# Kernel optimization log

Measured on AMD Instinct MI355X. Metric: run time of the kernel, lower is better.

## Reference

```python
import jax, jax.numpy as jnp
import numpy as np

WH, WW = 7, 7           # window height/width
N = WH * WW             # tokens per window = 49
C = 768                 # num_channels
H = 24                  # num_heads
D = C // H              # head_dim = 32
B = 1024                # total windows (batch * windows-per-image)
NW = 64                 # windows per image (shift_mask leading dim)
EPS = 1e-5


def _relative_position_index():
    # Mirrors the torch buffer construction in __init__.
    coords = np.stack(np.meshgrid(np.arange(WH), np.arange(WW), indexing='ij'))  # [2,WH,WW]
    cf = coords.reshape(2, -1)                          # [2,N]
    rel = cf[:, :, None] - cf[:, None, :]               # [2,N,N]
    rel = rel.transpose(1, 2, 0).copy()                 # [N,N,2]
    rel[:, :, 0] += WH - 1
    rel[:, :, 1] += WW - 1
    rel[:, :, 0] *= 2 * WW - 1
    return jnp.asarray(rel.sum(-1), dtype=jnp.int32)    # [N,N]


def setup_inputs() -> dict:
    key = jax.random.key(0)
    ks = jax.random.split(key, 6)
    x = jax.random.normal(ks[0], (B, N, C), dtype=jnp.float32)
    shift_mask = jax.random.normal(ks[1], (NW, N, N), dtype=jnp.float32)
    w_qkv = jax.random.normal(ks[2], (3 * C, C), dtype=jnp.float32) * 0.02
    b_qkv = jnp.zeros((3 * C,), dtype=jnp.float32)
    w_proj = jax.random.normal(ks[3], (C, C), dtype=jnp.float32) * 0.02
    b_proj = jnp.zeros((C,), dtype=jnp.float32)
    rel_bias_table = jax.random.normal(ks[4], ((2 * WH - 1) * (2 * WW - 1), H), dtype=jnp.float32) * 0.02
    ln_g = jnp.ones((C,), dtype=jnp.float32)
    ln_b = jnp.zeros((C,), dtype=jnp.float32)
    rel_pos_index = _relative_position_index()
    return {
        'x': x, 'shift_mask': shift_mask,
        'w_qkv': w_qkv, 'b_qkv': b_qkv,
        'w_proj': w_proj, 'b_proj': b_proj,
        'rel_bias_table': rel_bias_table,
        'ln_g': ln_g, 'ln_b': ln_b,
        'rel_pos_index': rel_pos_index,
    }


def reference(x, shift_mask, w_qkv, b_qkv, w_proj, b_proj, rel_bias_table, ln_g, ln_b, rel_pos_index):
    B_, N_, C_ = x.shape
    # QKV projection: [B,N,3C] -> [3,B,H,N,D]
    qkv = (x @ w_qkv.T + b_qkv).reshape(B_, N_, 3, H, D).transpose(2, 0, 3, 1, 4)
    q, k, v = qkv[0], qkv[1], qkv[2]
    # Relative position bias gather: [N,N,H] -> [1,H,N,N]
    bias = rel_bias_table[rel_pos_index.reshape(-1)].reshape(N_, N_, H).transpose(2, 0, 1)[None]
    # Shift mask broadcast over batch repeats and heads: [B,1,N,N]
    mask = jnp.tile(shift_mask, (B_ // shift_mask.shape[0], 1, 1))[:, None]
    attn_bias = bias + mask  # [B,H,N,N]
    scale = 1.0 / np.sqrt(D).astype(np.float32)
    scores = jnp.einsum('bhnd,bhmd->bhnm', q, k) * scale + attn_bias
    attn = jax.nn.softmax(scores, axis=-1)
    out = jnp.einsum('bhnm,bhmd->bhnd', attn, v)       # [B,H,N,D]
    out = out.transpose(0, 2, 1, 3).reshape(B_, N_, C_)
    out = out @ w_proj.T + b_proj                      # dropout p=0 -> identity
    y = out + x
    mu = jnp.mean(y, axis=-1, keepdims=True)
    var = jnp.mean(jnp.square(y - mu), axis=-1, keepdims=True)
    return (y - mu) * jax.lax.rsqrt(var + EPS) * ln_g + ln_b
```

## Files before the change

### kernel.cpp

```cpp
#include <hip/hip_runtime.h>
#include <hip/hip_bf16.h>

#define SEQ 49
#define CH 768
#define NH 24
#define HD 32
#define NB 1024
#define NWIN 64
#define MTOT (NB*SEQ)

typedef __hip_bfloat16 bf16;
typedef __attribute__((ext_vector_type(8))) short short8;
typedef __attribute__((ext_vector_type(4))) short short4v;
typedef __attribute__((ext_vector_type(4))) float f32x4;

#define MD  ((size_t)MTOT * HD)
#define NHMD ((size_t)NH * MD)

__device__ __forceinline__ void gload16(const void* g, void* l) {
  __builtin_amdgcn_global_load_lds((__attribute__((address_space(1))) void*)g,
                                   (__attribute__((address_space(3))) void*)l,
                                   16, 0, 0);
}

__device__ __forceinline__ float bf2f(short s) {
  return __uint_as_float(((unsigned int)(unsigned short)s) << 16);
}

__global__ void cvt_bf16(const float* __restrict__ in, bf16* __restrict__ o, int n4) {
  int i = blockIdx.x * blockDim.x + threadIdx.x;
  if (i >= n4) return;
  float4 v = ((const float4*)in)[i];
  union { bf16 b[4]; short4 s; } u;
  u.b[0] = __float2bfloat16(v.x);
  u.b[1] = __float2bfloat16(v.y);
  u.b[2] = __float2bfloat16(v.z);
  u.b[3] = __float2bfloat16(v.w);
  ((short4*)o)[i] = u.s;
}

__global__ void build_comb(const float* __restrict__ table, const int* __restrict__ rpi,
                           const float* __restrict__ smask, bf16* __restrict__ comb) {
  int i = blockIdx.x * blockDim.x + threadIdx.x;
  if (i >= NWIN * NH * 1024) return;
  int idx = i * 4;
  int e0 = idx & 7;
  int l = (idx >> 3) & 63;
  int jj = (idx >> 9) & 7;
  int sh = idx >> 12;
  int h = sh % NH;
  int s = sh / NH;
  union { bf16 b[4]; short4 v; } u;
#pragma unroll
  for (int k = 0; k < 4; k++) {
    int j = jj * 8 + e0 + k;
    int mt = j >> 4, nt = (j >> 2) & 3, r = j & 3;
    int m = 16 * mt + 4 * (l >> 4) + r;
    int n = 16 * nt + (l & 15);
    float v = -1e30f;
    if (m < SEQ && n < SEQ)
      v = (table[rpi[m * SEQ + n] * NH + h] + smask[s * SEQ * SEQ + m * SEQ + n])
          * 1.4426950408889634f;
    u.b[k] = __float2bfloat16(v);
  }
  *(short4*)(comb + idx) = u.v;
}

__global__ __launch_bounds__(512) void qkv_gemm(
    const bf16* __restrict__ A, const bf16* __restrict__ Bw,
    const float* __restrict__ bias, bf16* __restrict__ C)
{
  extern __shared__ __align__(16) bf16 lds[];
  const int tid = threadIdx.x;
  const int w = tid >> 6, l = tid & 63;
  const int lr = l & 15, lg = l >> 4;
  const int wm = w >> 2, wn = w & 3;

  const int flat = blockIdx.x;
  const int xcd = flat & 7, lid = flat >> 3;
  const int wgid = (xcd < 4 ? xcd * 221 : 884 + (xcd - 4) * 220) + lid;
  const int bm = wgid / 9, bn = wgid - 9 * bm;

  const bf16* gA[4];
  const bf16* gB[4];
  int ldst[4];
#pragma unroll
  for (int j = 0; j < 4; j++) {
    int c = j * 512 + tid;
    int row = c >> 3, cpos = c & 7;
    int srcch = cpos ^ (row & 7);
    gA[j] = A + ((size_t)(bm * 256 + row)) * CH + srcch * 8;
    gB[j] = Bw + ((size_t)(bn * 256 + row)) * CH + srcch * 8;
    ldst[j] = c * 8;
  }

  f32x4 acc[8][4];
  f32x4 zero4 = {0.f, 0.f, 0.f, 0.f};
#pragma unroll
  for (int i = 0; i < 8; i++)
#pragma unroll
    for (int j = 0; j < 4; j++) acc[i][j] = zero4;

  int offA[8][2], offB[4][2];
#pragma unroll
  for (int mi = 0; mi < 8; mi++)
#pragma unroll
    for (int ks = 0; ks < 2; ks++) {
      int rowa = wm * 128 + mi * 16 + lr;
      offA[mi][ks] = rowa * 64 + ((lg + 4 * ks) ^ (rowa & 7)) * 8;
    }
#pragma unroll
  for (int nj = 0; nj < 4; nj++)
#pragma unroll
    for (int ks = 0; ks < 2; ks++) {
      int rowb = wn * 64 + nj * 16 + lr;
      offB[nj][ks] = rowb * 64 + ((lg + 4 * ks) ^ (rowb & 7)) * 8;
    }

  gload16(gB[0], lds + 32768 + ldst[0]);
  gload16(gB[1], lds + 32768 + ldst[1]);
  gload16(gB[2], lds + 32768 + ldst[2]);
  gload16(gB[3], lds + 32768 + ldst[3]);
  gload16(gA[0], lds + ldst[0]);
  gload16(gA[2], lds + ldst[2]);
  gload16(gA[1], lds + ldst[1]);
  gload16(gA[3], lds + ldst[3]);

  for (int t = 0; t < 12; ++t) {
    const int cur = t & 1;
    const bf16* cA = lds + cur * 16384;
    const bf16* cB = lds + 32768 + cur * 16384;
    bf16* nA = lds + (cur ^ 1) * 16384;
    bf16* nB = lds + 32768 + (cur ^ 1) * 16384;
    const int kk = (t + 1) * 64;
    const bool pf = (t < 11);
#pragma unroll
    for (int p = 0; p < 4; ++p) {
      const int hp = p >> 1, ks = p & 1;
      if (p == 0) {
        asm volatile("s_waitcnt vmcnt(2)" ::: "memory");
      } else if (p == 2) {
        if (pf) asm volatile("s_waitcnt vmcnt(4)" ::: "memory");
        else    asm volatile("s_waitcnt vmcnt(0)" ::: "memory");
      }
      __builtin_amdgcn_sched_barrier(0);
      __builtin_amdgcn_s_barrier();
      __builtin_amdgcn_sched_barrier(0);
      short8 af[4], bfv[4];
#pragma unroll
      for (int mi = 0; mi < 4; mi++) af[mi] = *(const short8*)(cA + offA[hp * 4 + mi][ks]);
#pragma unroll
      for (int nj = 0; nj < 4; nj++) bfv[nj] = *(const short8*)(cB + offB[nj][ks]);
      if (pf) {
        if (p == 0) { gload16(gB[0] + kk, nB + ldst[0]); gload16(gB[1] + kk, nB + ldst[1]); }
        if (p == 1) { gload16(gB[2] + kk, nB + ldst[2]); gload16(gB[3] + kk, nB + ldst[3]); }
        if (p == 2) { gload16(gA[0] + kk, nA + ldst[0]); gload16(gA[2] + kk, nA + ldst[2]); }
        if (p == 3) { gload16(gA[1] + kk, nA + ldst[1]); gload16(gA[3] + kk, nA + ldst[3]); }
      }
      asm volatile("s_waitcnt lgkmcnt(0)" ::: "memory");
      __builtin_amdgcn_sched_barrier(0);
      __builtin_amdgcn_s_setprio(1);
#pragma unroll
      for (int mi = 0; mi < 4; mi++)
#pragma unroll
        for (int nj = 0; nj < 4; nj++)
          acc[hp * 4 + mi][nj] =
              __builtin_amdgcn_mfma_f32_16x16x32_bf16(af[mi], bfv[nj], acc[hp * 4 + mi][nj], 0, 0, 0);
      __builtin_amdgcn_s_setprio(0);
    }
  }

  const float scale = 0.25503487724583985f;
  const int colbase = bn * 256 + 64 * wn;
  const int rowbase = bm * 256 + 128 * wm;
#pragma unroll
  for (int nj = 0; nj < 4; nj++) {
    const int cb16 = colbase + 16 * nj;
    const int sec = cb16 / 768;
    const int rem = cb16 - sec * 768;
    const int h = rem >> 5;
    const int dbase = rem & 31;
    float bv = bias[cb16 + lr];
    if (sec == 2) {
      const size_t vbase = 2 * NHMD + ((size_t)h * HD + dbase + lr) * MTOT;
#pragma unroll
      for (int mi = 0; mi < 8; mi++) {
        size_t row = rowbase + 16 * mi + 4 * lg;
        union { bf16 b[4]; short4 s; } u;
#pragma unroll
        for (int r = 0; r < 4; r++) u.b[r] = __float2bfloat16(acc[mi][nj][r] + bv);
        *(short4*)(C + vbase + row) = u.s;
      }
    } else {
      const float mul = (sec == 0) ? scale : 1.0f;
      const size_t base = (size_t)sec * NHMD + (size_t)h * MD + dbase + lr;
#pragma unroll
      for (int mi = 0; mi < 8; mi++) {
#pragma unroll
        for (int r = 0; r < 4; r++) {
          size_t row = rowbase + 16 * mi + 4 * lg + r;
          C[base + row * HD] = __float2bfloat16((acc[mi][nj][r] + bv) * mul);
        }
      }
    }
  }
}

__global__ __launch_bounds__(256, 3) void attn_kernel(
    const bf16* __restrict__ qkvT, const bf16* __restrict__ comb,
    bf16* __restrict__ aout)
{
  __shared__ __align__(16) bf16 P[4][64 * 72];
  const int tid = threadIdx.x;
  const int w = tid >> 6, l = tid & 63;
  const int lr = l & 15, lg = l >> 4;
  const int b = blockIdx.x;
  const int h = blockIdx.y * 4 + w;
  const size_t rowb = (size_t)b * SEQ;
  f32x4 zero4 = {0.f, 0.f, 0.f, 0.f};

  const bf16* qb = qkvT + (size_t)h * MD + rowb * HD;
  const bf16* kb = qkvT + NHMD + (size_t)h * MD + rowb * HD;
  const bf16* vT = qkvT + 2 * NHMD + (size_t)h * HD * MTOT;

  short8 qf[4], kf[4];
#pragma unroll
  for (int mt = 0; mt < 4; mt++)
    qf[mt] = *(const short8*)(qb + (16 * mt + lr) * HD + 8 * lg);
#pragma unroll
  for (int nt = 0; nt < 4; nt++)
    kf[nt] = *(const short8*)(kb + (16 * nt + lr) * HD + 8 * lg);

  f32x4 s[4][4];
#pragma unroll
  for (int mt = 0; mt < 4; mt++)
#pragma unroll
    for (int nt = 0; nt < 4; nt++)
      s[mt][nt] = __builtin_amdgcn_mfma_f32_16x16x32_bf16(qf[mt], kf[nt], zero4, 0, 0, 0);

  short8 pb[2][2];
#pragma unroll
  for (int kt = 0; kt < 2; kt++)
#pragma unroll
    for (int dt = 0; dt < 2; dt++)
      pb[kt][dt] = *(const short8*)(vT + ((size_t)(16 * dt + lr)) * MTOT + rowb + 32 * kt + 8 * lg);

  const bf16* cbp = comb + (((size_t)(b & (NWIN - 1)) * NH + h) << 12);
  short8 c8[8];
#pragma unroll
  for (int jj = 0; jj < 8; jj++)
    c8[jj] = *(const short8*)(cbp + (jj * 64 + l) * 8);
#pragma unroll
  for (int jj = 0; jj < 8; jj++)
#pragma unroll
    for (int e = 0; e < 8; e++)
      s[jj >> 1][(jj & 1) * 2 + (e >> 2)][e & 3] += bf2f(c8[jj][e]);

  float inv[4][4];
#pragma unroll
  for (int mt = 0; mt < 4; mt++)
#pragma unroll
    for (int r = 0; r < 4; r++) {
      float t = 0.f;
#pragma unroll
      for (int nt = 0; nt < 4; nt++) {
        float e = exp2f(s[mt][nt][r]);
        s[mt][nt][r] = e;
        t += e;
      }
      t += __shfl_xor(t, 1, 64);
      t += __shfl_xor(t, 2, 64);
      t += __shfl_xor(t, 4, 64);
      t += __shfl_xor(t, 8, 64);
      inv[mt][r] = 1.0f / t;
    }

#pragma unroll
  for (int mt = 0; mt < 4; mt++)
#pragma unroll
    for (int nt = 0; nt < 4; nt++)
#pragma unroll
      for (int r = 0; r < 4; r++)
        P[w][(16 * mt + 4 * lg + r) * 72 + 16 * nt + lr] =
            __float2bfloat16(s[mt][nt][r]);

  f32x4 o[4][2];
#pragma unroll
  for (int mt = 0; mt < 4; mt++) { o[mt][0] = zero4; o[mt][1] = zero4; }
#pragma unroll
  for (int kt = 0; kt < 2; kt++) {
    short8 pa[4];
#pragma unroll
    for (int mt = 0; mt < 4; mt++)
      pa[mt] = *(const short8*)(&P[w][(16 * mt + lr) * 72 + 32 * kt + 8 * lg]);
#pragma unroll
    for (int mt = 0; mt < 4; mt++)
#pragma unroll
      for (int dt = 0; dt < 2; dt++)
        o[mt][dt] = __builtin_amdgcn_mfma_f32_16x16x32_bf16(pa[mt], pb[kt][dt], o[mt][dt], 0, 0, 0);
  }

#pragma unroll
  for (int mt = 0; mt < 4; mt++)
#pragma unroll
    for (int dt = 0; dt < 2; dt++)
#pragma unroll
      for (int r = 0; r < 4; r++) {
        int m = 16 * mt + 4 * lg + r;
        if (m < SEQ)
          aout[(rowb + m) * CH + h * HD + 16 * dt + lr] =
              __float2bfloat16(o[mt][dt][r] * inv[mt][r]);
      }
}

__global__ __launch_bounds__(256) void proj_gemm(
    const bf16* __restrict__ A, const bf16* __restrict__ Bw,
    const float* __restrict__ bias, const bf16* __restrict__ xb,
    bf16* __restrict__ Y)
{
  __shared__ __align__(16) bf16 As[2 * 128 * 64];
  __shared__ __align__(16) bf16 Bs[2 * 128 * 64];
  const int tid = threadIdx.x;
  const int w = tid >> 6, l = tid & 63;
  const int lr = l & 15, lg = l >> 4;
  const int wm = w >> 1, wn = w & 1;

  const int flat = blockIdx.x;
  const int wg = (flat & 7) * 294 + (flat >> 3);
  const int bm = wg / 6, bn = wg - 6 * (wg / 6);

  const bf16* gA[4];
  const bf16* gB[4];
  int ldst[4];
#pragma unroll
  for (int j = 0; j < 4; j++) {
    int c = j * 256 + tid;
    int row = c >> 3, cpos = c & 7;
    int srcch = cpos ^ (row & 7);
    gA[j] = A + ((size_t)(bm * 128 + row)) * CH + srcch * 8;
    gB[j] = Bw + ((size_t)(bn * 128 + row)) * CH + srcch * 8;
    ldst[j] = c * 8;
  }

  f32x4 acc[4][4];
  f32x4 zero4 = {0.f, 0.f, 0.f, 0.f};
#pragma unroll
  for (int i = 0; i < 4; i++)
#pragma unroll
    for (int j = 0; j < 4; j++) acc[i][j] = zero4;

  int offA[4][2], offB[4][2];
#pragma unroll
  for (int mi = 0; mi < 4; mi++) {
#pragma unroll
    for (int ks = 0; ks < 2; ks++) {
      int rowa = 64 * wm + 16 * mi + lr;
      offA[mi][ks] = rowa * 64 + ((lg + 4 * ks) ^ (rowa & 7)) * 8;
      int rowb = 64 * wn + 16 * mi + lr;
      offB[mi][ks] = rowb * 64 + ((lg + 4 * ks) ^ (rowb & 7)) * 8;
    }
  }

#pragma unroll
  for (int j = 0; j < 4; j++) gload16(gA[j], As + ldst[j]);
#pragma unroll
  for (int j = 0; j < 4; j++) gload16(gB[j], Bs + ldst[j]);

  for (int t = 0; t < 12; ++t) {
    const int base = (t & 1) * 8192;
    asm volatile("s_waitcnt vmcnt(0)" ::: "memory");
    __builtin_amdgcn_sched_barrier(0);
    __builtin_amdgcn_s_barrier();
    __builtin_amdgcn_sched_barrier(0);
    const bf16* cA = As + base;
    const bf16* cB = Bs + base;
    bf16* nA = As + (base ^ 8192);
    bf16* nB = Bs + (base ^ 8192);
    const int kk = (t + 1) * 64;
    const bool pf = (t < 11);
#pragma unroll
    for (int ks = 0; ks < 2; ks++) {
      short8 af[4], bfv[4];
#pragma unroll
      for (int mi = 0; mi < 4; mi++) {
        af[mi] = *(const short8*)(cA + offA[mi][ks]);
        bfv[mi] = *(const short8*)(cB + offB[mi][ks]);
      }
      if (pf) {
#pragma unroll
        for (int j = 0; j < 2; j++) {
          gload16(gA[ks * 2 + j] + kk, nA + ldst[ks * 2 + j]);
          gload16(gB[ks * 2 + j] + kk, nB + ldst[ks * 2 + j]);
        }
      }
      asm volatile("s_waitcnt lgkmcnt(0)" ::: "memory");
      __builtin_amdgcn_sched_barrier(0);
      __builtin_amdgcn_s_setprio(1);
#pragma unroll
      for (int mi = 0; mi < 4; mi++)
#pragma unroll
        for (int nj = 0; nj < 4; nj++)
          acc[mi][nj] = __builtin_amdgcn_mfma_f32_16x16x32_bf16(af[mi], bfv[nj], acc[mi][nj], 0, 0, 0);
      __builtin_amdgcn_s_setprio(0);
    }
  }

  const int colbase = bn * 128 + 64 * wn;
  const int rowbase = bm * 128 + 64 * wm;
#pragma unroll
  for (int nj = 0; nj < 4; nj++) {
    int col = colbase + 16 * nj + lr;
    float bv = bias[col];
#pragma unroll
    for (int mi = 0; mi < 4; mi++) {
#pragma unroll
      for (int r = 0; r < 4; r++) {
        size_t row = rowbase + 16 * mi + 4 * lg + r;
        float v = acc[mi][nj][r] + bv + bf2f(((const short*)xb)[row * CH + col]);
        Y[row * CH + col] = __float2bfloat16(v);
      }
    }
  }
}

__global__ __launch_bounds__(256) void ln_kernel(
    const bf16* __restrict__ Y, const float* __restrict__ g,
    const float* __restrict__ be, float* __restrict__ out)
{
  const int w = threadIdx.x >> 6, l = threadIdx.x & 63;
  const size_t r = (size_t)blockIdx.x * 4 + w;
  const bf16* yr = Y + r * CH;

  short8 a = *(const short8*)(yr + 8 * l);
  short4v b4 = *(const short4v*)(yr + 512 + 4 * l);
  float v[12];
#pragma unroll
  for (int j = 0; j < 8; j++) v[j] = bf2f(a[j]);
#pragma unroll
  for (int j = 0; j < 4; j++) v[8 + j] = bf2f(b4[j]);

  float s1 = 0.f, s2 = 0.f;
#pragma unroll
  for (int j = 0; j < 12; j++) { s1 += v[j]; s2 += v[j] * v[j]; }
#pragma unroll
  for (int m = 1; m <= 32; m <<= 1) {
    s1 += __shfl_xor(s1, m, 64);
    s2 += __shfl_xor(s2, m, 64);
  }
  float mu = s1 * (1.0f / 768.0f);
  float var = s2 * (1.0f / 768.0f) - mu * mu;
  float rs = rsqrtf(var + 1e-5f);

  float4 g0 = *(const float4*)(g + 8 * l);
  float4 g1 = *(const float4*)(g + 8 * l + 4);
  float4 g2 = *(const float4*)(g + 512 + 4 * l);
  float4 b0 = *(const float4*)(be + 8 * l);
  float4 b1 = *(const float4*)(be + 8 * l + 4);
  float4 b2 = *(const float4*)(be + 512 + 4 * l);

  float4 o0, o1, o2;
  o0.x = (v[0] - mu) * rs * g0.x + b0.x;
  o0.y = (v[1] - mu) * rs * g0.y + b0.y;
  o0.z = (v[2] - mu) * rs * g0.z + b0.z;
  o0.w = (v[3] - mu) * rs * g0.w + b0.w;
  o1.x = (v[4] - mu) * rs * g1.x + b1.x;
  o1.y = (v[5] - mu) * rs * g1.y + b1.y;
  o1.z = (v[6] - mu) * rs * g1.z + b1.z;
  o1.w = (v[7] - mu) * rs * g1.w + b1.w;
  o2.x = (v[8] - mu) * rs * g2.x + b2.x;
  o2.y = (v[9] - mu) * rs * g2.y + b2.y;
  o2.z = (v[10] - mu) * rs * g2.z + b2.z;
  o2.w = (v[11] - mu) * rs * g2.w + b2.w;

  float* orow = out + r * CH;
  *(float4*)(orow + 8 * l) = o0;
  *(float4*)(orow + 8 * l + 4) = o1;
  *(float4*)(orow + 512 + 4 * l) = o2;
}

extern "C" void kernel_launch(void* const* d_in, const int* in_sizes, int n_in,
                              void* d_out, int out_size, void* d_ws, size_t ws_size,
                              hipStream_t stream) {
  (void)in_sizes; (void)n_in; (void)out_size; (void)ws_size;
  const float* x     = (const float*)d_in[0];
  const float* smask = (const float*)d_in[1];
  const float* wqkv  = (const float*)d_in[2];
  const float* bqkv  = (const float*)d_in[3];
  const float* wproj = (const float*)d_in[4];
  const float* bproj = (const float*)d_in[5];
  const float* table = (const float*)d_in[6];
  const float* lng   = (const float*)d_in[7];
  const float* lnb   = (const float*)d_in[8];
  const int*   rpi   = (const int*)d_in[9];
  float* out = (float*)d_out;

  char* ws = (char*)d_ws;
  bf16*  xb   = (bf16*)(ws);
  bf16*  wqb  = (bf16*)(ws + 77070336);
  bf16*  wpb  = (bf16*)(ws + 80609280);
  bf16*  comb = (bf16*)(ws + 81788928);
  bf16*  qkvT = (bf16*)(ws + 94371840);
  bf16*  aout = (bf16*)(ws + 325582848);
  bf16*  yb   = (bf16*)(ws + 94371840);

  cvt_bf16<<<37632, 256, 0, stream>>>(x, xb, 9633792);
  cvt_bf16<<<1728, 256, 0, stream>>>(wqkv, wqb, 442368);
  cvt_bf16<<<576, 256, 0, stream>>>(wproj, wpb, 147456);
  build_comb<<<6144, 256, 0, stream>>>(table, rpi, smask, comb);
  qkv_gemm<<<1764, 512, 131072, stream>>>(xb, wqb, bqkv, qkvT);
  attn_kernel<<<dim3(1024, 6), 256, 0, stream>>>(qkvT, comb, aout);
  proj_gemm<<<2352, 256, 0, stream>>>(aout, wpb, bproj, xb, yb);
  ln_kernel<<<12544, 256, 0, stream>>>(yb, lng, lnb, out);
}
```

Measured before the change: 520.3 us.

## Stream attention score tiles per row-block and issue all GEMM prefetches up front

The attention kernel now computes QK^T, adds the bias/mask, runs the softmax and writes P one 16-row tile at a time, instead of holding the full 4x4 score array in registers. The launch bound rises from 3 to 4 blocks per SM. The aim is lower register pressure so more waves can be resident. In the GEMM main loop, all eight next-tile global-to-LDS loads are now issued in the first k-substep rather than split across both, so they start earlier. The cost is more load/MFMA serialization inside each tile step and a burstier memory queue.

```diff
diff --git a/kernel.cpp b/kernel.cpp
--- a/kernel.cpp
+++ b/kernel.cpp
@@ -206,7 +206,7 @@
   }
 }
 
-__global__ __launch_bounds__(256, 3) void attn_kernel(
+__global__ __launch_bounds__(256, 4) void attn_kernel(
     const bf16* __restrict__ qkvT, const bf16* __restrict__ comb,
     bf16* __restrict__ aout)
 {
@@ -223,21 +223,11 @@
   const bf16* kb = qkvT + NHMD + (size_t)h * MD + rowb * HD;
   const bf16* vT = qkvT + 2 * NHMD + (size_t)h * HD * MTOT;
 
-  short8 qf[4], kf[4];
-#pragma unroll
-  for (int mt = 0; mt < 4; mt++)
-    qf[mt] = *(const short8*)(qb + (16 * mt + lr) * HD + 8 * lg);
+  short8 kf[4];
 #pragma unroll
   for (int nt = 0; nt < 4; nt++)
     kf[nt] = *(const short8*)(kb + (16 * nt + lr) * HD + 8 * lg);
 
-  f32x4 s[4][4];
-#pragma unroll
-  for (int mt = 0; mt < 4; mt++)
-#pragma unroll
-    for (int nt = 0; nt < 4; nt++)
-      s[mt][nt] = __builtin_amdgcn_mfma_f32_16x16x32_bf16(qf[mt], kf[nt], zero4, 0, 0, 0);
-
   short8 pb[2][2];
 #pragma unroll
   for (int kt = 0; kt < 2; kt++)
@@ -246,26 +236,28 @@
       pb[kt][dt] = *(const short8*)(vT + ((size_t)(16 * dt + lr)) * MTOT + rowb + 32 * kt + 8 * lg);
 
   const bf16* cbp = comb + (((size_t)(b & (NWIN - 1)) * NH + h) << 12);
-  short8 c8[8];
-#pragma unroll
-  for (int jj = 0; jj < 8; jj++)
-    c8[jj] = *(const short8*)(cbp + (jj * 64 + l) * 8);
-#pragma unroll
-  for (int jj = 0; jj < 8; jj++)
-#pragma unroll
-    for (int e = 0; e < 8; e++)
-      s[jj >> 1][(jj & 1) * 2 + (e >> 2)][e & 3] += bf2f(c8[jj][e]);
-
   float inv[4][4];
-#pragma unroll
-  for (int mt = 0; mt < 4; mt++)
+
+#pragma unroll
+  for (int mt = 0; mt < 4; mt++) {
+    short8 qf = *(const short8*)(qb + (16 * mt + lr) * HD + 8 * lg);
+    f32x4 s4[4];
+#pragma unroll
+    for (int nt = 0; nt < 4; nt++)
+      s4[nt] = __builtin_amdgcn_mfma_f32_16x16x32_bf16(qf, kf[nt], zero4, 0, 0, 0);
+    short8 c0 = *(const short8*)(cbp + ((2 * mt) * 64 + l) * 8);
+    short8 c1 = *(const short8*)(cbp + ((2 * mt + 1) * 64 + l) * 8);
+#pragma unroll
+    for (int e = 0; e < 8; e++) s4[e >> 2][e & 3] += bf2f(c0[e]);
+#pragma unroll
+    for (int e = 0; e < 8; e++) s4[2 + (e >> 2)][e & 3] += bf2f(c1[e]);
 #pragma unroll
     for (int r = 0; r < 4; r++) {
       float t = 0.f;
 #pragma unroll
       for (int nt = 0; nt < 4; nt++) {
-        float e = exp2f(s[mt][nt][r]);
-        s[mt][nt][r] = e;
+        float e = exp2f(s4[nt][r]);
+        s4[nt][r] = e;
         t += e;
       }
       t += __shfl_xor(t, 1, 64);
@@ -274,15 +266,12 @@
       t += __shfl_xor(t, 8, 64);
       inv[mt][r] = 1.0f / t;
     }
-
-#pragma unroll
-  for (int mt = 0; mt < 4; mt++)
 #pragma unroll
     for (int nt = 0; nt < 4; nt++)
 #pragma unroll
       for (int r = 0; r < 4; r++)
-        P[w][(16 * mt + 4 * lg + r) * 72 + 16 * nt + lr] =
-            __float2bfloat16(s[mt][nt][r]);
+        P[w][(16 * mt + 4 * lg + r) * 72 + 16 * nt + lr] = __float2bfloat16(s4[nt][r]);
+  }
 
   f32x4 o[4][2];
 #pragma unroll
@@ -386,11 +375,11 @@
         af[mi] = *(const short8*)(cA + offA[mi][ks]);
         bfv[mi] = *(const short8*)(cB + offB[mi][ks]);
       }
-      if (pf) {
-#pragma unroll
-        for (int j = 0; j < 2; j++) {
-          gload16(gA[ks * 2 + j] + kk, nA + ldst[ks * 2 + j]);
-          gload16(gB[ks * 2 + j] + kk, nB + ldst[ks * 2 + j]);
+      if (pf && ks == 0) {
+#pragma unroll
+        for (int j = 0; j < 4; j++) {
+          gload16(gA[j] + kk, nA + ldst[j]);
+          gload16(gB[j] + kk, nB + ldst[j]);
         }
       }
       asm volatile("s_waitcnt lgkmcnt(0)" ::: "memory");
```

Result: no change. 512.7 us (median of 2 runs) (-1.4%).
